# Optimization experiments

Hardware: AMD Instinct MI355X
Metric: run time of the kernel (lower is better)

Reference implementation:

```python
import jax, jax.numpy as jnp
import numpy as np

KERNEL = 2
STRIDE = 2
N_QUBITS = 4
N_LAYERS = 2
PI = np.float32(np.pi)
EPS = np.float32(1e-8)


def setup_inputs() -> dict:
    key = jax.random.key(0)
    k1, k2, k3, k4 = jax.random.split(key, 4)
    x = jax.random.normal(k1, (64, 3, 512, 512), dtype=jnp.float32)
    weights = jax.random.normal(k2, (N_LAYERS, N_QUBITS, 3), dtype=jnp.float32) * 0.1
    proj_w = jax.random.normal(k3, (4, N_QUBITS, 1, 1), dtype=jnp.float32) * 0.5
    proj_b = jax.random.normal(k4, (4,), dtype=jnp.float32) * 0.1
    return {"x": x, "weights": weights, "proj_w": proj_w, "proj_b": proj_b}


def _extract_patches(x):
    # x: (B, C, H, W) -> flattened 2x2 patches of grayscale image: (B, Ho, Wo, 4)
    B, C, H, W = x.shape
    Ho = (H - KERNEL) // STRIDE + 1
    Wo = (W - KERNEL) // STRIDE + 1
    x_gray = x.mean(axis=1)  # (B, H, W)
    # stride == kernel, so non-overlapping patches via reshape
    p = x_gray.reshape(B, Ho, KERNEL, Wo, KERNEL)
    p = p.transpose(0, 1, 3, 2, 4).reshape(B, Ho, Wo, KERNEL * KERNEL)
    return p


def reference(x, weights, proj_w, proj_b):
    patches = _extract_patches(x)  # (B, Ho, Wo, 4)
    # global min-max normalization (matches patches.min()/max() over whole tensor)
    pmin = patches.min()
    pmax = patches.max()
    patches = (patches - pmin) / (pmax - pmin + EPS)

    # simplified quantum simulation, fully vectorized over (B, Ho, Wo)
    encoded = jnp.sin(patches * PI)  # (B, Ho, Wo, Q)
    for layer in range(N_LAYERS):
        w = weights[layer]  # (Q, 3)
        neighbor = jnp.roll(encoded, shift=-1, axis=-1)  # encoded[(i+1)%Q]
        mixed = encoded * jnp.cos(w[:, 0]) + neighbor * jnp.sin(w[:, 1]) + w[:, 2]
        encoded = jnp.tanh(mixed)

    # (B, Ho, Wo, Q) -> (B, Q, Ho, Wo), then 1x1 conv projection
    q = encoded.transpose(0, 3, 1, 2)
    out = jnp.einsum('bqhw,oq->bohw', q, proj_w[:, :, 0, 0]) + proj_b[None, :, None, None]
    return out
```

## Files before the change

kernel.cpp:

```cpp
#include <hip/hip_runtime.h>
#include <math.h>

constexpr int BN = 64, CH = 3, HH = 512, WW = 512;
constexpr int HO = 256, WO = 256;
constexpr int HW = HH * WW;
constexpr int HOWO = HO * WO;
constexpr float EPS_F = 1e-8f;

__device__ __forceinline__ void atomicMinF(float* a, float v) {
    if (v >= 0.0f) atomicMin((int*)a, __float_as_int(v));
    else           atomicMax((unsigned int*)a, __float_as_uint(v));
}
__device__ __forceinline__ void atomicMaxF(float* a, float v) {
    if (v >= 0.0f) atomicMax((int*)a, __float_as_int(v));
    else           atomicMin((unsigned int*)a, __float_as_uint(v));
}

__global__ void k_init(float* mm) {
    mm[0] = __int_as_float(0x7F800000);
    mm[1] = __int_as_float(0xFF800000);
}

__global__ __launch_bounds__(256) void k_minmax(const float* __restrict__ x,
                                                float* __restrict__ mm) {
    const int total4 = BN * HW / 4;
    const float c13 = 1.0f / 3.0f;
    float vmin = __int_as_float(0x7F800000);
    float vmax = __int_as_float(0xFF800000);
    for (int i = blockIdx.x * blockDim.x + threadIdx.x; i < total4;
         i += gridDim.x * blockDim.x) {
        int pix = i * 4;
        int b   = pix / HW;
        int rem = pix - b * HW;
        const float* base = x + b * (CH * HW) + rem;
        float4 a0 = *(const float4*)(base);
        float4 a1 = *(const float4*)(base + HW);
        float4 a2 = *(const float4*)(base + 2 * HW);
        float g0 = (a0.x + a1.x + a2.x) * c13;
        float g1 = (a0.y + a1.y + a2.y) * c13;
        float g2 = (a0.z + a1.z + a2.z) * c13;
        float g3 = (a0.w + a1.w + a2.w) * c13;
        vmin = fminf(vmin, fminf(fminf(g0, g1), fminf(g2, g3)));
        vmax = fmaxf(vmax, fmaxf(fmaxf(g0, g1), fmaxf(g2, g3)));
    }
    #pragma unroll
    for (int off = 32; off > 0; off >>= 1) {
        vmin = fminf(vmin, __shfl_down(vmin, off, 64));
        vmax = fmaxf(vmax, __shfl_down(vmax, off, 64));
    }
    __shared__ float smin[4], smax[4];
    int lane = threadIdx.x & 63, wid = threadIdx.x >> 6;
    if (lane == 0) { smin[wid] = vmin; smax[wid] = vmax; }
    __syncthreads();
    if (threadIdx.x == 0) {
        float m = smin[0], M = smax[0];
        #pragma unroll
        for (int i = 1; i < 4; ++i) { m = fminf(m, smin[i]); M = fmaxf(M, smax[i]); }
        atomicMinF(&mm[0], m);
        atomicMaxF(&mm[1], M);
    }
}

__device__ __forceinline__ float fast_tanh(float x) {
    float t = __builtin_amdgcn_exp2f(x * 2.8853900817779268f);
    return 1.0f - 2.0f * __builtin_amdgcn_rcpf(t + 1.0f);
}

__global__ __launch_bounds__(256) void k_main(const float* __restrict__ x,
                                              const float* __restrict__ wts,
                                              const float* __restrict__ pw,
                                              const float* __restrict__ pb,
                                              const float* __restrict__ mm,
                                              float* __restrict__ out) {
    const int WP = WO / 2;
    int idx = blockIdx.x * blockDim.x + threadIdx.x;
    int wp = idx % WP;
    int t  = idx / WP;
    int ho = t % HO;
    int b  = t / HO;

    float pmin = mm[0];
    float inv  = 1.0f / (mm[1] - pmin + EPS_F);
    float sscale = inv * 0.5f;

    const float inv2pi = 0.15915494309189535f;
    float c0[2][4], s1[2][4], b2[2][4];
    #pragma unroll
    for (int l = 0; l < 2; ++l)
        #pragma unroll
        for (int q = 0; q < 4; ++q) {
            c0[l][q] = __builtin_amdgcn_cosf(wts[(l * 4 + q) * 3 + 0] * inv2pi);
            s1[l][q] = __builtin_amdgcn_sinf(wts[(l * 4 + q) * 3 + 1] * inv2pi);
            b2[l][q] = wts[(l * 4 + q) * 3 + 2];
        }

    const float c13 = 1.0f / 3.0f;
    const float* xb = x + b * (CH * HW) + (2 * ho) * WW + 4 * wp;
    float4 r0c0 = *(const float4*)(xb);
    float4 r1c0 = *(const float4*)(xb + WW);
    float4 r0c1 = *(const float4*)(xb + HW);
    float4 r1c1 = *(const float4*)(xb + HW + WW);
    float4 r0c2 = *(const float4*)(xb + 2 * HW);
    float4 r1c2 = *(const float4*)(xb + 2 * HW + WW);

    float g0x = (r0c0.x + r0c1.x + r0c2.x) * c13;
    float g0y = (r0c0.y + r0c1.y + r0c2.y) * c13;
    float g0z = (r0c0.z + r0c1.z + r0c2.z) * c13;
    float g0w = (r0c0.w + r0c1.w + r0c2.w) * c13;
    float g1x = (r1c0.x + r1c1.x + r1c2.x) * c13;
    float g1y = (r1c0.y + r1c1.y + r1c2.y) * c13;
    float g1z = (r1c0.z + r1c1.z + r1c2.z) * c13;
    float g1w = (r1c0.w + r1c1.w + r1c2.w) * c13;

    float e[2][4];
    e[0][0] = g0x; e[0][1] = g0y; e[0][2] = g1x; e[0][3] = g1y;
    e[1][0] = g0z; e[1][1] = g0w; e[1][2] = g1z; e[1][3] = g1w;

    #pragma unroll
    for (int p = 0; p < 2; ++p) {
        #pragma unroll
        for (int q = 0; q < 4; ++q)
            e[p][q] = __builtin_amdgcn_sinf((e[p][q] - pmin) * sscale);
        #pragma unroll
        for (int l = 0; l < 2; ++l) {
            float m[4];
            #pragma unroll
            for (int q = 0; q < 4; ++q)
                m[q] = e[p][q] * c0[l][q] + e[p][(q + 1) & 3] * s1[l][q] + b2[l][q];
            #pragma unroll
            for (int q = 0; q < 4; ++q)
                e[p][q] = fast_tanh(m[q]);
        }
    }

    int obase = b * (4 * HOWO) + ho * WO + 2 * wp;
    #pragma unroll
    for (int o = 0; o < 4; ++o) {
        float w0 = pw[o * 4 + 0], w1 = pw[o * 4 + 1], w2 = pw[o * 4 + 2], w3 = pw[o * 4 + 3];
        float2 v;
        v.x = pb[o] + e[0][0] * w0 + e[0][1] * w1 + e[0][2] * w2 + e[0][3] * w3;
        v.y = pb[o] + e[1][0] * w0 + e[1][1] * w1 + e[1][2] * w2 + e[1][3] * w3;
        *(float2*)(out + obase + o * HOWO) = v;
    }
}

extern "C" void kernel_launch(void* const* d_in, const int* in_sizes, int n_in,
                              void* d_out, int out_size, void* d_ws, size_t ws_size,
                              hipStream_t stream) {
    const float* x   = (const float*)d_in[0];
    const float* wts = (const float*)d_in[1];
    const float* pw  = (const float*)d_in[2];
    const float* pb  = (const float*)d_in[3];
    float* out = (float*)d_out;
    float* mm  = (float*)d_ws;

    k_init<<<1, 1, 0, stream>>>(mm);
    k_minmax<<<2048, 256, 0, stream>>>(x, mm);
    const int threads = BN * HO * (WO / 2);
    k_main<<<threads / 256, 256, 0, stream>>>(x, wts, pw, pb, mm, out);
}
```

Before: 338.6 us.

## Cache grayscale as fp16 in workspace to avoid rereading input in main pass

The first pass now computes the channel-mean grayscale once, stores it as packed fp16 in workspace, and writes per-block min/max partials. A single-block kernel reduces those partials in place of the atomics. The main kernel then reads only the compact fp16 grayscale instead of rereading all three fp32 channels, and each thread handles four output pixels with float4 stores. This cuts global memory traffic, but the fp16 rounding of grayscale values adds error before normalization.

```diff
diff --git a/kernel.cpp b/kernel.cpp
--- a/kernel.cpp
+++ b/kernel.cpp
@@ -1,5 +1,5 @@
 #include <hip/hip_runtime.h>
-#include <math.h>
+#include <hip/hip_fp16.h>
 
 constexpr int BN = 64, CH = 3, HH = 512, WW = 512;
 constexpr int HO = 256, WO = 256;
@@ -7,81 +7,125 @@
 constexpr int HOWO = HO * WO;
 constexpr float EPS_F = 1e-8f;
 
-__device__ __forceinline__ void atomicMinF(float* a, float v) {
-    if (v >= 0.0f) atomicMin((int*)a, __float_as_int(v));
-    else           atomicMax((unsigned int*)a, __float_as_uint(v));
-}
-__device__ __forceinline__ void atomicMaxF(float* a, float v) {
-    if (v >= 0.0f) atomicMax((int*)a, __float_as_int(v));
-    else           atomicMin((unsigned int*)a, __float_as_uint(v));
-}
-
-__global__ void k_init(float* mm) {
-    mm[0] = __int_as_float(0x7F800000);
-    mm[1] = __int_as_float(0xFF800000);
-}
-
-__global__ __launch_bounds__(256) void k_minmax(const float* __restrict__ x,
-                                                float* __restrict__ mm) {
-    const int total4 = BN * HW / 4;
+constexpr int TPB = 256;
+constexpr int GROUPS = BN * HO * (WO / 4);
+constexpr int ABLOCKS = 2048;
+constexpr int AT = ABLOCKS * TPB;
+constexpr int AITERS = GROUPS / AT;
+constexpr int CBLOCKS = GROUPS / TPB;
+
+constexpr size_t GRAY_HALFS = (size_t)GROUPS * 16;
+
+__device__ __forceinline__ float fast_tanh(float x) {
+    float t = __builtin_amdgcn_exp2f(x * 2.8853900817779268f);
+    return 1.0f - 2.0f * __builtin_amdgcn_rcpf(t + 1.0f);
+}
+
+__global__ __launch_bounds__(TPB) void k_pass1(const float* __restrict__ x,
+                                               float4* __restrict__ gray4,
+                                               float* __restrict__ part) {
+    const int tid = blockIdx.x * TPB + threadIdx.x;
     const float c13 = 1.0f / 3.0f;
     float vmin = __int_as_float(0x7F800000);
     float vmax = __int_as_float(0xFF800000);
-    for (int i = blockIdx.x * blockDim.x + threadIdx.x; i < total4;
-         i += gridDim.x * blockDim.x) {
-        int pix = i * 4;
-        int b   = pix / HW;
-        int rem = pix - b * HW;
-        const float* base = x + b * (CH * HW) + rem;
-        float4 a0 = *(const float4*)(base);
-        float4 a1 = *(const float4*)(base + HW);
-        float4 a2 = *(const float4*)(base + 2 * HW);
-        float g0 = (a0.x + a1.x + a2.x) * c13;
-        float g1 = (a0.y + a1.y + a2.y) * c13;
-        float g2 = (a0.z + a1.z + a2.z) * c13;
-        float g3 = (a0.w + a1.w + a2.w) * c13;
-        vmin = fminf(vmin, fminf(fminf(g0, g1), fminf(g2, g3)));
-        vmax = fmaxf(vmax, fmaxf(fmaxf(g0, g1), fmaxf(g2, g3)));
-    }
+
+    #pragma unroll
+    for (int it = 0; it < AITERS; ++it) {
+        int grp = it * AT + tid;
+        int b   = grp >> 14;
+        int rem = grp & 16383;
+        int ho  = rem >> 6;
+        int wp  = rem & 63;
+        const float* base = x + b * (CH * HW) + (2 * ho) * WW + 8 * wp;
+
+        float row0[8], row1[8];
+        #pragma unroll
+        for (int c = 0; c < CH; ++c) {
+            const float* pc = base + c * HW;
+            float4 u0 = *(const float4*)(pc);
+            float4 u1 = *(const float4*)(pc + 4);
+            float4 v0 = *(const float4*)(pc + WW);
+            float4 v1 = *(const float4*)(pc + WW + 4);
+            float uu[8] = {u0.x, u0.y, u0.z, u0.w, u1.x, u1.y, u1.z, u1.w};
+            float vv[8] = {v0.x, v0.y, v0.z, v0.w, v1.x, v1.y, v1.z, v1.w};
+            if (c == 0) {
+                #pragma unroll
+                for (int k = 0; k < 8; ++k) { row0[k] = uu[k]; row1[k] = vv[k]; }
+            } else {
+                #pragma unroll
+                for (int k = 0; k < 8; ++k) { row0[k] += uu[k]; row1[k] += vv[k]; }
+            }
+        }
+        #pragma unroll
+        for (int k = 0; k < 8; ++k) {
+            row0[k] *= c13; row1[k] *= c13;
+            vmin = fminf(vmin, fminf(row0[k], row1[k]));
+            vmax = fmaxf(vmax, fmaxf(row0[k], row1[k]));
+        }
+        alignas(16) __half2 h2[8];
+        #pragma unroll
+        for (int p = 0; p < 4; ++p) {
+            h2[2 * p]     = __floats2half2_rn(row0[2 * p], row0[2 * p + 1]);
+            h2[2 * p + 1] = __floats2half2_rn(row1[2 * p], row1[2 * p + 1]);
+        }
+        gray4[(size_t)grp * 2]     = *(const float4*)&h2[0];
+        gray4[(size_t)grp * 2 + 1] = *(const float4*)&h2[4];
+    }
+
     #pragma unroll
     for (int off = 32; off > 0; off >>= 1) {
         vmin = fminf(vmin, __shfl_down(vmin, off, 64));
         vmax = fmaxf(vmax, __shfl_down(vmax, off, 64));
     }
-    __shared__ float smin[4], smax[4];
+    __shared__ float sm[8];
     int lane = threadIdx.x & 63, wid = threadIdx.x >> 6;
-    if (lane == 0) { smin[wid] = vmin; smax[wid] = vmax; }
+    if (lane == 0) { sm[wid] = vmin; sm[4 + wid] = vmax; }
     __syncthreads();
     if (threadIdx.x == 0) {
-        float m = smin[0], M = smax[0];
-        #pragma unroll
-        for (int i = 1; i < 4; ++i) { m = fminf(m, smin[i]); M = fmaxf(M, smax[i]); }
-        atomicMinF(&mm[0], m);
-        atomicMaxF(&mm[1], M);
-    }
-}
-
-__device__ __forceinline__ float fast_tanh(float x) {
-    float t = __builtin_amdgcn_exp2f(x * 2.8853900817779268f);
-    return 1.0f - 2.0f * __builtin_amdgcn_rcpf(t + 1.0f);
-}
-
-__global__ __launch_bounds__(256) void k_main(const float* __restrict__ x,
+        part[2 * blockIdx.x]     = fminf(fminf(sm[0], sm[1]), fminf(sm[2], sm[3]));
+        part[2 * blockIdx.x + 1] = fmaxf(fmaxf(sm[4], sm[5]), fmaxf(sm[6], sm[7]));
+    }
+}
+
+__global__ __launch_bounds__(TPB) void k_reduce(const float* __restrict__ part,
+                                                float* __restrict__ mm) {
+    float m = __int_as_float(0x7F800000);
+    float M = __int_as_float(0xFF800000);
+    #pragma unroll
+    for (int i = 0; i < ABLOCKS / TPB; ++i) {
+        int j = i * TPB + threadIdx.x;
+        m = fminf(m, part[2 * j]);
+        M = fmaxf(M, part[2 * j + 1]);
+    }
+    #pragma unroll
+    for (int off = 32; off > 0; off >>= 1) {
+        m = fminf(m, __shfl_down(m, off, 64));
+        M = fmaxf(M, __shfl_down(M, off, 64));
+    }
+    __shared__ float sm[8];
+    int lane = threadIdx.x & 63, wid = threadIdx.x >> 6;
+    if (lane == 0) { sm[wid] = m; sm[4 + wid] = M; }
+    __syncthreads();
+    if (threadIdx.x == 0) {
+        mm[0] = fminf(fminf(sm[0], sm[1]), fminf(sm[2], sm[3]));
+        mm[1] = fmaxf(fmaxf(sm[4], sm[5]), fmaxf(sm[6], sm[7]));
+    }
+}
+
+__global__ __launch_bounds__(TPB) void k_main(const float4* __restrict__ gray4,
                                               const float* __restrict__ wts,
                                               const float* __restrict__ pw,
                                               const float* __restrict__ pb,
                                               const float* __restrict__ mm,
                                               float* __restrict__ out) {
-    const int WP = WO / 2;
-    int idx = blockIdx.x * blockDim.x + threadIdx.x;
-    int wp = idx % WP;
-    int t  = idx / WP;
-    int ho = t % HO;
-    int b  = t / HO;
-
-    float pmin = mm[0];
-    float inv  = 1.0f / (mm[1] - pmin + EPS_F);
-    float sscale = inv * 0.5f;
+    int grp = blockIdx.x * TPB + threadIdx.x;
+    int b   = grp >> 14;
+    int rem = grp & 16383;
+    int ho  = rem >> 6;
+    int wp  = rem & 63;
+
+    float pmin   = mm[0];
+    float sscale = 0.5f / (mm[1] - pmin + EPS_F);
 
     const float inv2pi = 0.15915494309189535f;
     float c0[2][4], s1[2][4], b2[2][4];
@@ -93,54 +137,54 @@
             s1[l][q] = __builtin_amdgcn_sinf(wts[(l * 4 + q) * 3 + 1] * inv2pi);
             b2[l][q] = wts[(l * 4 + q) * 3 + 2];
         }
-
-    const float c13 = 1.0f / 3.0f;
-    const float* xb = x + b * (CH * HW) + (2 * ho) * WW + 4 * wp;
-    float4 r0c0 = *(const float4*)(xb);
-    float4 r1c0 = *(const float4*)(xb + WW);
-    float4 r0c1 = *(const float4*)(xb + HW);
-    float4 r1c1 = *(const float4*)(xb + HW + WW);
-    float4 r0c2 = *(const float4*)(xb + 2 * HW);
-    float4 r1c2 = *(const float4*)(xb + 2 * HW + WW);
-
-    float g0x = (r0c0.x + r0c1.x + r0c2.x) * c13;
-    float g0y = (r0c0.y + r0c1.y + r0c2.y) * c13;
-    float g0z = (r0c0.z + r0c1.z + r0c2.z) * c13;
-    float g0w = (r0c0.w + r0c1.w + r0c2.w) * c13;
-    float g1x = (r1c0.x + r1c1.x + r1c2.x) * c13;
-    float g1y = (r1c0.y + r1c1.y + r1c2.y) * c13;
-    float g1z = (r1c0.z + r1c1.z + r1c2.z) * c13;
-    float g1w = (r1c0.w + r1c1.w + r1c2.w) * c13;
-
-    float e[2][4];
-    e[0][0] = g0x; e[0][1] = g0y; e[0][2] = g1x; e[0][3] = g1y;
-    e[1][0] = g0z; e[1][1] = g0w; e[1][2] = g1z; e[1][3] = g1w;
-
-    #pragma unroll
-    for (int p = 0; p < 2; ++p) {
+    float pwr[4][4], pbr[4];
+    #pragma unroll
+    for (int o = 0; o < 4; ++o) {
+        pbr[o] = pb[o];
+        #pragma unroll
+        for (int q = 0; q < 4; ++q) pwr[o][q] = pw[o * 4 + q];
+    }
+
+    alignas(16) __half2 h2[8];
+    *(float4*)&h2[0] = gray4[(size_t)grp * 2];
+    *(float4*)&h2[4] = gray4[(size_t)grp * 2 + 1];
+
+    float e[4][4];
+    #pragma unroll
+    for (int p = 0; p < 4; ++p) {
+        e[p][0] = __low2float(h2[2 * p]);     e[p][1] = __high2float(h2[2 * p]);
+        e[p][2] = __low2float(h2[2 * p + 1]); e[p][3] = __high2float(h2[2 * p + 1]);
+    }
+    #pragma unroll
+    for (int p = 0; p < 4; ++p)
         #pragma unroll
         for (int q = 0; q < 4; ++q)
             e[p][q] = __builtin_amdgcn_sinf((e[p][q] - pmin) * sscale);
-        #pragma unroll
-        for (int l = 0; l < 2; ++l) {
-            float m[4];
+    #pragma unroll
+    for (int l = 0; l < 2; ++l)
+        #pragma unroll
+        for (int p = 0; p < 4; ++p) {
+            float mq[4];
             #pragma unroll
             for (int q = 0; q < 4; ++q)
-                m[q] = e[p][q] * c0[l][q] + e[p][(q + 1) & 3] * s1[l][q] + b2[l][q];
+                mq[q] = e[p][q] * c0[l][q] + e[p][(q + 1) & 3] * s1[l][q] + b2[l][q];
             #pragma unroll
-            for (int q = 0; q < 4; ++q)
-                e[p][q] = fast_tanh(m[q]);
-        }
-    }
-
-    int obase = b * (4 * HOWO) + ho * WO + 2 * wp;
+            for (int q = 0; q < 4; ++q) e[p][q] = fast_tanh(mq[q]);
+        }
+
+    float* ob = out + b * (4 * HOWO) + ho * WO + 4 * wp;
     #pragma unroll
     for (int o = 0; o < 4; ++o) {
-        float w0 = pw[o * 4 + 0], w1 = pw[o * 4 + 1], w2 = pw[o * 4 + 2], w3 = pw[o * 4 + 3];
-        float2 v;
-        v.x = pb[o] + e[0][0] * w0 + e[0][1] * w1 + e[0][2] * w2 + e[0][3] * w3;
-        v.y = pb[o] + e[1][0] * w0 + e[1][1] * w1 + e[1][2] * w2 + e[1][3] * w3;
-        *(float2*)(out + obase + o * HOWO) = v;
+        float4 v;
+        float* vp = &v.x;
+        #pragma unroll
+        for (int p = 0; p < 4; ++p) {
+            float acc = pbr[o];
+            #pragma unroll
+            for (int q = 0; q < 4; ++q) acc += e[p][q] * pwr[o][q];
+            vp[p] = acc;
+        }
+        *(float4*)(ob + o * HOWO) = v;
     }
 }
 
@@ -152,10 +196,12 @@
     const float* pw  = (const float*)d_in[2];
     const float* pb  = (const float*)d_in[3];
     float* out = (float*)d_out;
-    float* mm  = (float*)d_ws;
-
-    k_init<<<1, 1, 0, stream>>>(mm);
-    k_minmax<<<2048, 256, 0, stream>>>(x, mm);
-    const int threads = BN * HO * (WO / 2);
-    k_main<<<threads / 256, 256, 0, stream>>>(x, wts, pw, pb, mm, out);
-}
+
+    float4* gray4 = (float4*)d_ws;
+    float*  part  = (float*)((char*)d_ws + GRAY_HALFS * sizeof(__half));
+    float*  mm    = part + 2 * ABLOCKS;
+
+    k_pass1 <<<ABLOCKS, TPB, 0, stream>>>(x, gray4, part);
+    k_reduce<<<1,       TPB, 0, stream>>>(part, mm);
+    k_main  <<<CBLOCKS, TPB, 0, stream>>>(gray4, wts, pw, pb, mm, out);
+}
```

Measured after the change: 314.1 us. 7.2% less time.
